# Optimization experiments

Measured on AMD Instinct MI355X. Metric: run time of the kernel, lower is better.

## Reference

```python
import jax, jax.numpy as jnp
import numpy as np

N = 50000      # nodes
E = 800000     # edges
IN_DIM = 16
D = 128        # latent_dim == d_model == num_heads*d_head
H = 8
DH = 16
DFF = 512
L = 3          # n_layers
CLAMP = 5.0
EPS = 1e-5


def _layer_norm(x, g, b):
    mu = jnp.mean(x, axis=-1, keepdims=True)
    var = jnp.mean((x - mu) ** 2, axis=-1, keepdims=True)
    return (x - mu) * jax.lax.rsqrt(var + EPS) * g + b


def setup_inputs() -> dict:
    key = jax.random.key(0)
    ks = jax.random.split(key, 16)
    def w(k, shape, fan_in):
        return jax.random.normal(k, shape, dtype=jnp.float32) * (1.0 / np.sqrt(fan_in))
    inp = {
        "nf": jax.random.normal(ks[0], (N, IN_DIM), dtype=jnp.float32),
        "src": jax.random.randint(ks[1], (E,), 0, N, dtype=jnp.int32),
        "dst": jax.random.randint(ks[2], (E,), 0, N, dtype=jnp.int32),
        "enc_W": w(ks[3], (D, IN_DIM), IN_DIM),
        "enc_b": jnp.zeros((D,), jnp.float32),
        "Wq": w(ks[4], (L, H * DH, D), D),
        "Wk": w(ks[5], (L, H * DH, D), D),
        "Wv": w(ks[6], (L, H * DH, D), D),
        "Wo": w(ks[7], (L, D, H * DH), H * DH),
        "ln1_g": jnp.ones((L, D), jnp.float32),
        "ln1_b": jnp.zeros((L, D), jnp.float32),
        "ffn_W1": w(ks[8], (L, DFF, D), D),
        "ffn_b1": jnp.zeros((L, DFF), jnp.float32),
        "ffn_W2": w(ks[9], (L, D, DFF), DFF),
        "ffn_b2": jnp.zeros((L, D), jnp.float32),
        "ln2_g": jnp.ones((L, D), jnp.float32),
        "ln2_b": jnp.zeros((L, D), jnp.float32),
        "dec_W": w(ks[10], (1, D), D),
        "dec_b": jnp.zeros((1,), jnp.float32),
    }
    return inp


def reference(nf, src, dst, enc_W, enc_b, Wq, Wk, Wv, Wo, ln1_g, ln1_b,
              ffn_W1, ffn_b1, ffn_W2, ffn_b2, ln2_g, ln2_b, dec_W, dec_b):
    h = nf @ enc_W.T + enc_b                       # [N, D]
    scale = 1.0 / np.sqrt(DH)
    for l in range(L):
        q = h @ Wq[l].T                            # [N, H*DH]
        k = h @ Wk[l].T
        v = h @ Wv[l].T
        qe = q[dst].reshape(E, H, DH)              # per-edge gather (dst query)
        ke = k[src].reshape(E, H, DH)
        u = jnp.sum(qe * ke, axis=-1) * scale      # [E, H]
        u = jnp.clip(u, -CLAMP, CLAMP)
        # edge_softmax: normalize over edges sharing the same dst node
        m = jax.ops.segment_max(u, dst, num_segments=N)   # [N, H]
        e = jnp.exp(u - m[dst])
        s = jax.ops.segment_sum(e, dst, num_segments=N)   # [N, H]
        a = e / s[dst]                             # [E, H]
        av = a[..., None] * v[src].reshape(E, H, DH)      # [E, H, DH]
        sum_av = jax.ops.segment_sum(av.reshape(E, H * DH), dst, num_segments=N)
        uh = sum_av @ Wo[l].T                      # [N, D]
        h1 = _layer_norm(h + uh, ln1_g[l], ln1_b[l])
        f = jax.nn.relu(h1 @ ffn_W1[l].T + ffn_b1[l]) @ ffn_W2[l].T + ffn_b2[l]
        h = _layer_norm(h1 + f, ln2_g[l], ln2_b[l])
    pred = h @ dec_W.T + dec_b                     # [N, 1]
    # BasicReadout('mean') over the single batched graph -> [1, 1]
    return jnp.mean(pred, axis=0, keepdims=True)
```

## Files before the change

kernel.cpp:

```cpp
#include <hip/hip_runtime.h>
#include <math.h>

static constexpr int D   = 128;
static constexpr int DFF = 512;
static constexpr int LAYERS = 3;
static constexpr float CLAMP_V = 5.0f;
static constexpr float LN_EPS = 1e-5f;

typedef unsigned short u16;
typedef unsigned int   u32;
typedef short bf16x8 __attribute__((ext_vector_type(8)));
typedef float f32x4  __attribute__((ext_vector_type(4)));

__device__ inline float4 ld4(const float* p){ return *reinterpret_cast<const float4*>(p); }
__device__ inline u16 f2bf(float f){ u32 u = __float_as_uint(f); return (u16)((u + 0x7fff + ((u>>16)&1)) >> 16); }
__device__ inline float bl(u32 u){ return __uint_as_float(u << 16); }
__device__ inline float bh(u32 u){ return __uint_as_float(u & 0xffff0000u); }

__device__ inline void gload_lds16(const void* g, void* l) {
  __builtin_amdgcn_global_load_lds(
      (const __attribute__((address_space(1))) void*)g,
      (__attribute__((address_space(3))) void*)l, 16, 0, 0);
}

__global__ __launch_bounds__(256) void count_kernel(const int* __restrict__ dst,
                                                    int* __restrict__ deg, int E)
{
  int e = blockIdx.x*256 + threadIdx.x;
  if (e < E) atomicAdd(&deg[dst[e]], 1);
}

__global__ __launch_bounds__(256) void scan_bsum(const int* __restrict__ deg,
                                                 int* __restrict__ bsum, int N)
{
  const int i0 = blockIdx.x*1024 + threadIdx.x*4;
  int s = 0;
  if (i0 + 3 < N) { int4 v = *(const int4*)&deg[i0]; s = v.x+v.y+v.z+v.w; }
  else { for (int t = 0; t < 4; t++) if (i0+t < N) s += deg[i0+t]; }
  #pragma unroll
  for (int off = 1; off < 64; off <<= 1) s += __shfl_xor(s, off);
  __shared__ int ws_[4];
  if ((threadIdx.x & 63) == 0) ws_[threadIdx.x >> 6] = s;
  __syncthreads();
  if (threadIdx.x == 0) bsum[blockIdx.x] = ws_[0]+ws_[1]+ws_[2]+ws_[3];
}

__global__ __launch_bounds__(64) void scan_bbase(int* __restrict__ bsum, int NB)
{
  const int tid = threadIdx.x;
  int base = 0;
  for (int c = 0; c < NB; c += 64) {
    const int idx = c + tid;
    int v = (idx < NB) ? bsum[idx] : 0;
    const int orig = v;
    #pragma unroll
    for (int off = 1; off < 64; off <<= 1) {
      int t = __shfl_up(v, off);
      if (tid >= off) v += t;
    }
    if (idx < NB) bsum[idx] = base + v - orig;
    base += __shfl(v, 63);
  }
}

__global__ __launch_bounds__(256) void scan_write(const int* __restrict__ deg,
    const int* __restrict__ bbase, int* __restrict__ offs, int* __restrict__ cursor, int N)
{
  const int i0 = blockIdx.x*1024 + threadIdx.x*4;
  int v[4] = {0,0,0,0};
  if (i0 + 3 < N) { int4 t = *(const int4*)&deg[i0]; v[0]=t.x; v[1]=t.y; v[2]=t.z; v[3]=t.w; }
  else { for (int t = 0; t < 4; t++) if (i0+t < N) v[t] = deg[i0+t]; }
  const int s = v[0]+v[1]+v[2]+v[3];
  const int lane = threadIdx.x & 63, w = threadIdx.x >> 6;
  int inc = s;
  #pragma unroll
  for (int off = 1; off < 64; off <<= 1) {
    int t = __shfl_up(inc, off);
    if (lane >= off) inc += t;
  }
  __shared__ int wsum[4];
  if (lane == 63) wsum[w] = inc;
  __syncthreads();
  int wb = 0;
  for (int t = 0; t < 4; t++) if (t < w) wb += wsum[t];
  int run = bbase[blockIdx.x] + wb + inc - s;
  #pragma unroll
  for (int t = 0; t < 4; t++) {
    if (i0 + t < N) { offs[i0+t] = run; cursor[i0+t] = run; run += v[t]; }
  }
  if (i0 <= N-1 && N-1 < i0+4) offs[N] = run;
}

__global__ __launch_bounds__(256) void fill_kernel(const int* __restrict__ dst,
    const int* __restrict__ src, int* __restrict__ cursor, int* __restrict__ csr_src, int E)
{
  int e = blockIdx.x*256 + threadIdx.x;
  if (e < E) {
    int p = atomicAdd(&cursor[dst[e]], 1);
    csr_src[p] = src[e];
  }
}

__global__ __launch_bounds__(256) void convert_weights(
    const float* __restrict__ Wq, const float* __restrict__ Wk, const float* __restrict__ Wv,
    const float* __restrict__ Wo, const float* __restrict__ W1, const float* __restrict__ W2,
    u16* __restrict__ out)
{
  const int SQKV = 3*384*128;
  const int SWO  = 3*128*128;
  const int SW1  = 3*512*128;
  const int SW2  = 3*128*512;
  int i = blockIdx.x*256 + threadIdx.x;
  if (i >= SQKV+SWO+SW1+SW2) return;
  float v;
  if (i < SQKV) {
    int l = i / (384*128), rem = i % (384*128);
    int row = rem / 128, col = rem % 128;
    const float* W = (row < 128) ? Wq : ((row < 256) ? Wk : Wv);
    v = W[(size_t)l*128*128 + (size_t)(row & 127)*128 + col];
  } else if (i < SQKV+SWO) {
    v = Wo[i - SQKV];
  } else if (i < SQKV+SWO+SW1) {
    v = W1[i - SQKV - SWO];
  } else {
    v = W2[i - SQKV - SWO - SW1];
  }
  out[i] = f2bf(v);
}

__global__ __launch_bounds__(256) void encoder_kernel(
    const float* __restrict__ nf, const float* __restrict__ W,
    const float* __restrict__ b, float* __restrict__ h, u16* __restrict__ hb, int N)
{
  int n = blockIdx.x*2 + (threadIdx.x >> 7);
  int d = threadIdx.x & 127;
  if (n >= N) return;
  const float* nr = nf + (size_t)n*16;
  const float* wr = W  + (size_t)d*16;
  float s = b[d];
  #pragma unroll
  for (int kk = 0; kk < 16; kk++) s = fmaf(nr[kk], wr[kk], s);
  h[(size_t)n*D + d]  = s;
  hb[(size_t)n*D + d] = f2bf(s);
}

template<int K>
__device__ inline void gemm_core(const u16* __restrict__ A, const u16* __restrict__ B,
                                 int M, int m0, u16* lA, u16* lB, f32x4 acc[4][4])
{
  const int tid  = threadIdx.x;
  const int lane = tid & 63;
  const int wid  = tid >> 6;
  const int wr   = wid >> 1, wc = wid & 1;

  const int ldrow = lane >> 3;
  const int gran  = (lane & 7) ^ ldrow;

  #pragma unroll
  for (int ks = 0; ks < K/64; ks++) {
    __syncthreads();
    const int k0 = ks*64 + gran*8;
    #pragma unroll
    for (int is = 0; is < 4; is++) {
      const int r  = wid*32 + is*8;
      int gm = m0 + r + ldrow; if (gm >= M) gm = M - 1;
      gload_lds16(A + (size_t)gm*K + k0, &lA[r*64]);
      gload_lds16(B + (size_t)(r + ldrow)*K + k0, &lB[r*64]);
    }
    asm volatile("s_waitcnt vmcnt(0)" ::: "memory");
    __syncthreads();

    #pragma unroll
    for (int k2 = 0; k2 < 2; k2++) {
      bf16x8 af[4], bfr[4];
      const int kq = k2*4 + (lane >> 4);
      #pragma unroll
      for (int mi = 0; mi < 4; mi++) {
        const int r = wr*64 + mi*16 + (lane & 15);
        af[mi] = *(const bf16x8*)&lA[r*64 + ((kq ^ (r & 7)) << 3)];
      }
      #pragma unroll
      for (int ni = 0; ni < 4; ni++) {
        const int r = wc*64 + ni*16 + (lane & 15);
        bfr[ni] = *(const bf16x8*)&lB[r*64 + ((kq ^ (r & 7)) << 3)];
      }
      #pragma unroll
      for (int mi = 0; mi < 4; mi++)
        #pragma unroll
        for (int ni = 0; ni < 4; ni++)
          acc[mi][ni] = __builtin_amdgcn_mfma_f32_16x16x32_bf16(af[mi], bfr[ni], acc[mi][ni], 0, 0, 0);
    }
  }
}

__global__ __launch_bounds__(256) void gemm_qkv(
    const u16* __restrict__ A, const u16* __restrict__ B,
    float* __restrict__ qf, u16* __restrict__ kvb, int M)
{
  __shared__ u16 lA[128*64];
  __shared__ u16 lB[128*64];
  const int s  = blockIdx.y;
  const int m0 = blockIdx.x * 128;
  f32x4 acc[4][4];
  #pragma unroll
  for (int i = 0; i < 4; i++)
    #pragma unroll
    for (int j = 0; j < 4; j++) { acc[i][j][0]=0.f; acc[i][j][1]=0.f; acc[i][j][2]=0.f; acc[i][j][3]=0.f; }

  gemm_core<128>(A, B + (size_t)s*128*128, M, m0, lA, lB, acc);

  const int lane  = threadIdx.x & 63;
  const int wid   = threadIdx.x >> 6;
  const int wr    = wid >> 1, wc = wid & 1;
  const int rbase = m0 + wr*64 + ((lane >> 4) << 2);
  const int cbase = wc*64 + (lane & 15);
  #pragma unroll
  for (int ni = 0; ni < 4; ni++) {
    const int col = cbase + ni*16;
    #pragma unroll
    for (int mi = 0; mi < 4; mi++) {
      #pragma unroll
      for (int r = 0; r < 4; r++) {
        const int gm = rbase + mi*16 + r;
        if (gm < M) {
          if (s == 0) qf[(size_t)gm*128 + col] = acc[mi][ni][r];
          else        kvb[(size_t)gm*256 + (s-1)*128 + col] = f2bf(acc[mi][ni][r]);
        }
      }
    }
  }
}

__global__ __launch_bounds__(256) void ffn_fused(
    const u16* __restrict__ savb, const u16* __restrict__ Wo,
    const u16* __restrict__ W1,   const u16* __restrict__ W2,
    const float* __restrict__ ln1g, const float* __restrict__ ln1b,
    const float* __restrict__ b1,   const float* __restrict__ b2,
    const float* __restrict__ ln2g, const float* __restrict__ ln2b,
    float* __restrict__ hf, u16* __restrict__ hb, int M)
{
  __shared__ u16 lA[64*64];
  __shared__ u16 lB[128*64];
  __shared__ u16 h1s[64*128];
  __shared__ u16 fs[64*128];
  __shared__ float lsum[64][2];
  __shared__ float lsq[64][2];

  const int tid  = threadIdx.x;
  const int lane = tid & 63;
  const int wid  = tid >> 6;
  const int wr   = wid >> 1, wc = wid & 1;
  const int m0   = blockIdx.x * 64;

  const int ldrow = lane >> 3;
  const int gran  = (lane & 7) ^ ldrow;

  const int rbase_l = wr*32 + ((lane >> 4) << 2);
  const int cbase   = wc*64 + (lane & 15);

  f32x4 acc1[2][4];
  #pragma unroll
  for (int i = 0; i < 2; i++)
    #pragma unroll
    for (int j = 0; j < 4; j++) { acc1[i][j][0]=0.f; acc1[i][j][1]=0.f; acc1[i][j][2]=0.f; acc1[i][j][3]=0.f; }

  #pragma unroll
  for (int ks = 0; ks < 2; ks++) {
    __syncthreads();
    const int k0 = ks*64 + gran*8;
    #pragma unroll
    for (int is = 0; is < 2; is++) {
      const int r = wid*16 + is*8;
      int gm = m0 + r + ldrow; if (gm >= M) gm = M - 1;
      gload_lds16(savb + (size_t)gm*128 + k0, &lA[r*64]);
    }
    #pragma unroll
    for (int is = 0; is < 4; is++) {
      const int r = wid*32 + is*8;
      gload_lds16(Wo + (size_t)(r + ldrow)*128 + k0, &lB[r*64]);
    }
    asm volatile("s_waitcnt vmcnt(0)" ::: "memory");
    __syncthreads();
    #pragma unroll
    for (int k2 = 0; k2 < 2; k2++) {
      const int kq = k2*4 + (lane >> 4);
      bf16x8 af[2], bfr[4];
      #pragma unroll
      for (int mi = 0; mi < 2; mi++) {
        const int r = wr*32 + mi*16 + (lane & 15);
        af[mi] = *(const bf16x8*)&lA[r*64 + ((kq ^ (r & 7)) << 3)];
      }
      #pragma unroll
      for (int ni = 0; ni < 4; ni++) {
        const int r = wc*64 + ni*16 + (lane & 15);
        bfr[ni] = *(const bf16x8*)&lB[r*64 + ((kq ^ (r & 7)) << 3)];
      }
      #pragma unroll
      for (int mi = 0; mi < 2; mi++)
        #pragma unroll
        for (int ni = 0; ni < 4; ni++)
          acc1[mi][ni] = __builtin_amdgcn_mfma_f32_16x16x32_bf16(af[mi], bfr[ni], acc1[mi][ni], 0, 0, 0);
    }
  }

  #pragma unroll
  for (int mi = 0; mi < 2; mi++) {
    #pragma unroll
    for (int r = 0; r < 4; r++) {
      const int lrow = rbase_l + mi*16 + r;
      int gr = m0 + lrow; if (gr >= M) gr = M - 1;
      float ps = 0.f, pq = 0.f;
      #pragma unroll
      for (int ni = 0; ni < 4; ni++) {
        const int col = cbase + ni*16;
        float x = acc1[mi][ni][r] + hf[(size_t)gr*128 + col];
        acc1[mi][ni][r] = x;
        ps += x; pq += x*x;
      }
      #pragma unroll
      for (int off = 1; off < 16; off <<= 1) { ps += __shfl_xor(ps, off); pq += __shfl_xor(pq, off); }
      if ((lane & 15) == 0) { lsum[lrow][wc] = ps; lsq[lrow][wc] = pq; }
    }
  }
  __syncthreads();
  #pragma unroll
  for (int mi = 0; mi < 2; mi++) {
    #pragma unroll
    for (int r = 0; r < 4; r++) {
      const int lrow = rbase_l + mi*16 + r;
      const float mean = (lsum[lrow][0] + lsum[lrow][1]) * (1.0f/128.0f);
      float var = (lsq[lrow][0] + lsq[lrow][1]) * (1.0f/128.0f) - mean*mean;
      const float rstd = rsqrtf(fmaxf(var, 0.f) + LN_EPS);
      #pragma unroll
      for (int ni = 0; ni < 4; ni++) {
        const int col = cbase + ni*16;
        float o = (acc1[mi][ni][r] - mean) * rstd * ln1g[col] + ln1b[col];
        acc1[mi][ni][r] = o;
        const int g16 = col >> 3;
        const int slot = ((g16 & 7) ^ (lrow & 7)) | (g16 & 8);
        h1s[lrow*128 + slot*8 + (col & 7)] = f2bf(o);
      }
    }
  }

  f32x4 acc3[2][4];
  #pragma unroll
  for (int i = 0; i < 2; i++)
    #pragma unroll
    for (int j = 0; j < 4; j++) { acc3[i][j][0]=0.f; acc3[i][j][1]=0.f; acc3[i][j][2]=0.f; acc3[i][j][3]=0.f; }

  for (int c = 0; c < 4; c++) {
    f32x4 acc2[2][4];
    #pragma unroll
    for (int i = 0; i < 2; i++)
      #pragma unroll
      for (int j = 0; j < 4; j++) { acc2[i][j][0]=0.f; acc2[i][j][1]=0.f; acc2[i][j][2]=0.f; acc2[i][j][3]=0.f; }

    #pragma unroll
    for (int s = 0; s < 2; s++) {
      __syncthreads();
      const int k0 = s*64 + gran*8;
      #pragma unroll
      for (int is = 0; is < 4; is++) {
        const int r = wid*32 + is*8;
        gload_lds16(W1 + (size_t)(c*128 + r + ldrow)*128 + k0, &lB[r*64]);
      }
      asm volatile("s_waitcnt vmcnt(0)" ::: "memory");
      __syncthreads();
      #pragma unroll
      for (int k2 = 0; k2 < 2; k2++) {
        const int kql = k2*4 + (lane >> 4);
        const int kqa = s*8 + kql;
        bf16x8 af[2], bfr[4];
        #pragma unroll
        for (int mi = 0; mi < 2; mi++) {
          const int r = wr*32 + mi*16 + (lane & 15);
          const int slot = ((kqa & 7) ^ (r & 7)) | (kqa & 8);
          af[mi] = *(const bf16x8*)&h1s[r*128 + slot*8];
        }
        #pragma unroll
        for (int ni = 0; ni < 4; ni++) {
          const int r = wc*64 + ni*16 + (lane & 15);
          bfr[ni] = *(const bf16x8*)&lB[r*64 + ((kql ^ (r & 7)) << 3)];
        }
        #pragma unroll
        for (int mi = 0; mi < 2; mi++)
          #pragma unroll
          for (int ni = 0; ni < 4; ni++)
            acc2[mi][ni] = __builtin_amdgcn_mfma_f32_16x16x32_bf16(af[mi], bfr[ni], acc2[mi][ni], 0, 0, 0);
      }
    }
    __syncthreads();
    #pragma unroll
    for (int mi = 0; mi < 2; mi++) {
      #pragma unroll
      for (int r = 0; r < 4; r++) {
        const int lrow = rbase_l + mi*16 + r;
        #pragma unroll
        for (int ni = 0; ni < 4; ni++) {
          const int col = cbase + ni*16;
          float v = fmaxf(acc2[mi][ni][r] + b1[c*128 + col], 0.f);
          const int g16 = col >> 3;
          const int slot = ((g16 & 7) ^ (lrow & 7)) | (g16 & 8);
          fs[lrow*128 + slot*8 + (col & 7)] = f2bf(v);
        }
      }
    }

    #pragma unroll
    for (int s = 0; s < 2; s++) {
      __syncthreads();
      const int k0 = s*64 + gran*8;
      #pragma unroll
      for (int is = 0; is < 4; is++) {
        const int r = wid*32 + is*8;
        gload_lds16(W2 + (size_t)(r + ldrow)*512 + c*128 + k0, &lB[r*64]);
      }
      asm volatile("s_waitcnt vmcnt(0)" ::: "memory");
      __syncthreads();
      #pragma unroll
      for (int k2 = 0; k2 < 2; k2++) {
        const int kql = k2*4 + (lane >> 4);
        const int kqa = s*8 + kql;
        bf16x8 af[2], bfr[4];
        #pragma unroll
        for (int mi = 0; mi < 2; mi++) {
          const int r = wr*32 + mi*16 + (lane & 15);
          const int slot = ((kqa & 7) ^ (r & 7)) | (kqa & 8);
          af[mi] = *(const bf16x8*)&fs[r*128 + slot*8];
        }
        #pragma unroll
        for (int ni = 0; ni < 4; ni++) {
          const int r = wc*64 + ni*16 + (lane & 15);
          bfr[ni] = *(const bf16x8*)&lB[r*64 + ((kql ^ (r & 7)) << 3)];
        }
        #pragma unroll
        for (int mi = 0; mi < 2; mi++)
          #pragma unroll
          for (int ni = 0; ni < 4; ni++)
            acc3[mi][ni] = __builtin_amdgcn_mfma_f32_16x16x32_bf16(af[mi], bfr[ni], acc3[mi][ni], 0, 0, 0);
      }
    }
  }

  #pragma unroll
  for (int mi = 0; mi < 2; mi++) {
    #pragma unroll
    for (int r = 0; r < 4; r++) {
      const int lrow = rbase_l + mi*16 + r;
      float ps = 0.f, pq = 0.f;
      #pragma unroll
      for (int ni = 0; ni < 4; ni++) {
        const int col = cbase + ni*16;
        float x = acc3[mi][ni][r] + b2[col] + acc1[mi][ni][r];
        acc3[mi][ni][r] = x;
        ps += x; pq += x*x;
      }
      #pragma unroll
      for (int off = 1; off < 16; off <<= 1) { ps += __shfl_xor(ps, off); pq += __shfl_xor(pq, off); }
      if ((lane & 15) == 0) { lsum[lrow][wc] = ps; lsq[lrow][wc] = pq; }
    }
  }
  __syncthreads();
  #pragma unroll
  for (int mi = 0; mi < 2; mi++) {
    #pragma unroll
    for (int r = 0; r < 4; r++) {
      const int lrow = rbase_l + mi*16 + r;
      const int grow = m0 + lrow;
      if (grow >= M) continue;
      const float mean = (lsum[lrow][0] + lsum[lrow][1]) * (1.0f/128.0f);
      float var = (lsq[lrow][0] + lsq[lrow][1]) * (1.0f/128.0f) - mean*mean;
      const float rstd = rsqrtf(fmaxf(var, 0.f) + LN_EPS);
      #pragma unroll
      for (int ni = 0; ni < 4; ni++) {
        const int col = cbase + ni*16;
        float o = (acc3[mi][ni][r] - mean) * rstd * ln2g[col] + ln2b[col];
        hf[(size_t)grow*128 + col] = o;
        hb[(size_t)grow*128 + col] = f2bf(o);
      }
    }
  }
}

__global__ __launch_bounds__(256) void attn_kernel(
    const float* __restrict__ q, const u16* __restrict__ kv,
    const int* __restrict__ offs, const int* __restrict__ csr_src,
    u16* __restrict__ outb, int N)
{
  const int tid = threadIdx.x;
  const int j   = tid & 15;
  const int n   = blockIdx.x*16 + (tid >> 4);
  if (n >= N) return;

  float qreg[8];
  *(float4*)&qreg[0] = ld4(&q[(size_t)n*128 + j*8]);
  *(float4*)&qreg[4] = ld4(&q[(size_t)n*128 + j*8 + 4]);

  const int start = offs[n];
  const int deg   = offs[n+1] - start;

  float s = 0.f;
  float acc[8] = {0,0,0,0,0,0,0,0};
  const int gb = tid & 48;

  for (int base = 0; base < deg; base += 16) {
    const int myidx = base + j;
    const int sn_mine = (myidx < deg) ? csr_src[start + myidx] : 0;
    const int cnt = (deg - base < 16) ? (deg - base) : 16;

    for (int b2 = 0; b2 < cnt; b2 += 4) {
      const int m4 = cnt - b2;
      uint4 K4[4], V4[4];
      #pragma unroll
      for (int u = 0; u < 4; u++) {
        const int sel = b2 + ((u < m4) ? u : 0);
        const int sn = __shfl(sn_mine, gb + sel);
        const u16* row = kv + (size_t)sn*256 + j*8;
        K4[u] = *(const uint4*)row;
        V4[u] = *(const uint4*)(row + 128);
      }
      #pragma unroll
      for (int u = 0; u < 4; u++) {
        if (u < m4) {
          float d = bl(K4[u].x)*qreg[0] + bh(K4[u].x)*qreg[1]
                  + bl(K4[u].y)*qreg[2] + bh(K4[u].y)*qreg[3]
                  + bl(K4[u].z)*qreg[4] + bh(K4[u].z)*qreg[5]
                  + bl(K4[u].w)*qreg[6] + bh(K4[u].w)*qreg[7];
          d += __shfl_xor(d, 1);
          float uu = fminf(fmaxf(d * 0.25f, -CLAMP_V), CLAMP_V);
          float e = __expf(uu - CLAMP_V);
          s += e;
          acc[0] = fmaf(e, bl(V4[u].x), acc[0]);
          acc[1] = fmaf(e, bh(V4[u].x), acc[1]);
          acc[2] = fmaf(e, bl(V4[u].y), acc[2]);
          acc[3] = fmaf(e, bh(V4[u].y), acc[3]);
          acc[4] = fmaf(e, bl(V4[u].z), acc[4]);
          acc[5] = fmaf(e, bh(V4[u].z), acc[5]);
          acc[6] = fmaf(e, bl(V4[u].w), acc[6]);
          acc[7] = fmaf(e, bh(V4[u].w), acc[7]);
        }
      }
    }
  }

  const float rs = (deg > 0) ? (1.0f / s) : 0.f;
  u16 o[8];
  #pragma unroll
  for (int t = 0; t < 8; t++) o[t] = f2bf(acc[t] * rs);
  *(uint4*)&outb[(size_t)n*128 + j*8] = *(const uint4*)o;
}

__global__ __launch_bounds__(256) void dec_partial(const float* __restrict__ h,
    const float* __restrict__ W, float* __restrict__ partials, int N)
{
  float acc = 0.f;
  for (int n = blockIdx.x*256 + threadIdx.x; n < N; n += 256*256) {
    const float* hr = h + (size_t)n*D;
    float s = 0.f;
    #pragma unroll
    for (int t = 0; t < 32; t++) {
      float4 hv = ld4(&hr[t*4]); float4 wv = ld4(&W[t*4]);
      s += hv.x*wv.x + hv.y*wv.y + hv.z*wv.z + hv.w*wv.w;
    }
    acc += s;
  }
  #pragma unroll
  for (int off = 1; off < 64; off <<= 1) acc += __shfl_xor(acc, off);
  __shared__ float red[4];
  int lane = threadIdx.x & 63, w = threadIdx.x >> 6;
  if (lane == 0) red[w] = acc;
  __syncthreads();
  if (threadIdx.x == 0) partials[blockIdx.x] = red[0]+red[1]+red[2]+red[3];
}

__global__ __launch_bounds__(256) void dec_final(const float* __restrict__ partials,
    const float* __restrict__ decb, float* __restrict__ out, int N)
{
  float a = partials[threadIdx.x];
  #pragma unroll
  for (int off = 1; off < 64; off <<= 1) a += __shfl_xor(a, off);
  __shared__ float red[4];
  int lane = threadIdx.x & 63, w = threadIdx.x >> 6;
  if (lane == 0) red[w] = a;
  __syncthreads();
  if (threadIdx.x == 0) out[0] = (red[0]+red[1]+red[2]+red[3]) / (float)N + decb[0];
}

extern "C" void kernel_launch(void* const* d_in, const int* in_sizes, int n_in,
                              void* d_out, int out_size, void* d_ws, size_t ws_size,
                              hipStream_t stream)
{
  const float* nf   = (const float*)d_in[0];
  const int*   src  = (const int*)  d_in[1];
  const int*   dst  = (const int*)  d_in[2];
  const float* encW = (const float*)d_in[3];
  const float* encb = (const float*)d_in[4];
  const float* Wq   = (const float*)d_in[5];
  const float* Wk   = (const float*)d_in[6];
  const float* Wv   = (const float*)d_in[7];
  const float* Wo   = (const float*)d_in[8];
  const float* ln1g = (const float*)d_in[9];
  const float* ln1b = (const float*)d_in[10];
  const float* W1   = (const float*)d_in[11];
  const float* b1   = (const float*)d_in[12];
  const float* W2   = (const float*)d_in[13];
  const float* b2   = (const float*)d_in[14];
  const float* ln2g = (const float*)d_in[15];
  const float* ln2b = (const float*)d_in[16];
  const float* decW = (const float*)d_in[17];
  const float* decb = (const float*)d_in[18];
  float* out = (float*)d_out;

  const int N = in_sizes[0] / 16;
  const int E = in_sizes[1];
  const int NB = (N + 1023) / 1024;

  float* ws   = (float*)d_ws;
  float* h    = ws;
  float* q    = h  + (size_t)N*128;
  u16*  hb    = (u16*)(q + (size_t)N*128);
  u16*  kvb   = hb  + (size_t)N*128;
  u16*  savb  = kvb + (size_t)N*256;
  int* deg    = (int*)(savb + (size_t)N*128);
  int* offs   = deg + N;
  int* cursor = offs + N + 1;
  int* csr    = cursor + N;
  int* bsum   = csr + E;
  float* partials = (float*)(bsum + ((NB + 255) & ~255));
  u16* wbuf   = (u16*)(partials + 512);
  u16* wqkv   = wbuf;
  u16* wo_b   = wbuf + 147456;
  u16* w1_b   = wbuf + 196608;
  u16* w2_b   = wbuf + 393216;

  hipMemsetAsync(deg, 0, sizeof(int)*N, stream);
  count_kernel<<<(E+255)/256, 256, 0, stream>>>(dst, deg, E);
  scan_bsum<<<NB, 256, 0, stream>>>(deg, bsum, N);
  scan_bbase<<<1, 64, 0, stream>>>(bsum, NB);
  scan_write<<<NB, 256, 0, stream>>>(deg, bsum, offs, cursor, N);
  fill_kernel<<<(E+255)/256, 256, 0, stream>>>(dst, src, cursor, csr, E);

  convert_weights<<<(589824+255)/256, 256, 0, stream>>>(Wq, Wk, Wv, Wo, W1, W2, wbuf);

  encoder_kernel<<<(N+1)/2, 256, 0, stream>>>(nf, encW, encb, h, hb, N);

  const int gmx = (N + 127)/128;
  for (int l = 0; l < LAYERS; l++) {
    const u16* wqkv_l = wqkv + (size_t)l*384*128;
    const u16* wo_l   = wo_b + (size_t)l*128*128;
    const u16* w1_l   = w1_b + (size_t)l*512*128;
    const u16* w2_l   = w2_b + (size_t)l*128*512;

    gemm_qkv<<<dim3(gmx,3), 256, 0, stream>>>(hb, wqkv_l, q, kvb, N);

    attn_kernel<<<(N+15)/16, 256, 0, stream>>>(q, kvb, offs, csr, savb, N);

    ffn_fused<<<(N+63)/64, 256, 0, stream>>>(
        savb, wo_l, w1_l, w2_l,
        ln1g + l*D, ln1b + l*D, b1 + l*DFF, b2 + l*D, ln2g + l*D, ln2b + l*D,
        h, hb, N);
  }

  dec_partial<<<256, 256, 0, stream>>>(h, decW, partials, N);
  dec_final<<<1, 256, 0, stream>>>(partials, decb, out, N);
}
```

Baseline: 567.6 us.

## Double-buffer LDS loads in QKV and FFN GEMMs; widen edge gather batch

```diff
diff --git a/kernel.cpp b/kernel.cpp
--- a/kernel.cpp
+++ b/kernel.cpp
@@ -144,52 +144,55 @@
   hb[(size_t)n*D + d] = f2bf(s);
 }
 
-template<int K>
-__device__ inline void gemm_core(const u16* __restrict__ A, const u16* __restrict__ B,
-                                 int M, int m0, u16* lA, u16* lB, f32x4 acc[4][4])
-{
-  const int tid  = threadIdx.x;
-  const int lane = tid & 63;
-  const int wid  = tid >> 6;
-  const int wr   = wid >> 1, wc = wid & 1;
-
-  const int ldrow = lane >> 3;
-  const int gran  = (lane & 7) ^ ldrow;
-
-  #pragma unroll
-  for (int ks = 0; ks < K/64; ks++) {
-    __syncthreads();
-    const int k0 = ks*64 + gran*8;
-    #pragma unroll
-    for (int is = 0; is < 4; is++) {
-      const int r  = wid*32 + is*8;
-      int gm = m0 + r + ldrow; if (gm >= M) gm = M - 1;
-      gload_lds16(A + (size_t)gm*K + k0, &lA[r*64]);
-      gload_lds16(B + (size_t)(r + ldrow)*K + k0, &lB[r*64]);
-    }
-    asm volatile("s_waitcnt vmcnt(0)" ::: "memory");
-    __syncthreads();
-
-    #pragma unroll
-    for (int k2 = 0; k2 < 2; k2++) {
-      bf16x8 af[4], bfr[4];
-      const int kq = k2*4 + (lane >> 4);
-      #pragma unroll
-      for (int mi = 0; mi < 4; mi++) {
-        const int r = wr*64 + mi*16 + (lane & 15);
-        af[mi] = *(const bf16x8*)&lA[r*64 + ((kq ^ (r & 7)) << 3)];
-      }
-      #pragma unroll
-      for (int ni = 0; ni < 4; ni++) {
-        const int r = wc*64 + ni*16 + (lane & 15);
-        bfr[ni] = *(const bf16x8*)&lB[r*64 + ((kq ^ (r & 7)) << 3)];
-      }
-      #pragma unroll
-      for (int mi = 0; mi < 4; mi++)
-        #pragma unroll
-        for (int ni = 0; ni < 4; ni++)
-          acc[mi][ni] = __builtin_amdgcn_mfma_f32_16x16x32_bf16(af[mi], bfr[ni], acc[mi][ni], 0, 0, 0);
-    }
+__device__ inline void mfma_step128(const u16* __restrict__ la, const u16* __restrict__ lb,
+                                    int lane, int wr, int wc, f32x4 (&acc)[4][4])
+{
+  #pragma unroll
+  for (int k2 = 0; k2 < 2; k2++) {
+    bf16x8 af[4], bfr[4];
+    const int kq = k2*4 + (lane >> 4);
+    #pragma unroll
+    for (int mi = 0; mi < 4; mi++) {
+      const int r = wr*64 + mi*16 + (lane & 15);
+      af[mi] = *(const bf16x8*)&la[r*64 + ((kq ^ (r & 7)) << 3)];
+    }
+    #pragma unroll
+    for (int ni = 0; ni < 4; ni++) {
+      const int r = wc*64 + ni*16 + (lane & 15);
+      bfr[ni] = *(const bf16x8*)&lb[r*64 + ((kq ^ (r & 7)) << 3)];
+    }
+    #pragma unroll
+    for (int mi = 0; mi < 4; mi++)
+      #pragma unroll
+      for (int ni = 0; ni < 4; ni++)
+        acc[mi][ni] = __builtin_amdgcn_mfma_f32_16x16x32_bf16(af[mi], bfr[ni], acc[mi][ni], 0, 0, 0);
+  }
+}
+
+__device__ inline void mfma_stage64(const u16* __restrict__ Atile, const u16* __restrict__ Btile,
+                                    int lane, int wr, int wc, int kabase, f32x4 (&acc)[2][4])
+{
+  #pragma unroll
+  for (int k2 = 0; k2 < 2; k2++) {
+    const int kql = k2*4 + (lane >> 4);
+    const int kqa = kabase + kql;
+    bf16x8 af[2], bfr[4];
+    #pragma unroll
+    for (int mi = 0; mi < 2; mi++) {
+      const int r = wr*32 + mi*16 + (lane & 15);
+      const int slot = ((kqa & 7) ^ (r & 7)) | (kqa & 8);
+      af[mi] = *(const bf16x8*)&Atile[r*128 + slot*8];
+    }
+    #pragma unroll
+    for (int ni = 0; ni < 4; ni++) {
+      const int r = wc*64 + ni*16 + (lane & 15);
+      bfr[ni] = *(const bf16x8*)&Btile[r*64 + ((kql ^ (r & 7)) << 3)];
+    }
+    #pragma unroll
+    for (int mi = 0; mi < 2; mi++)
+      #pragma unroll
+      for (int ni = 0; ni < 4; ni++)
+        acc[mi][ni] = __builtin_amdgcn_mfma_f32_16x16x32_bf16(af[mi], bfr[ni], acc[mi][ni], 0, 0, 0);
   }
 }
 
@@ -197,21 +200,42 @@
     const u16* __restrict__ A, const u16* __restrict__ B,
     float* __restrict__ qf, u16* __restrict__ kvb, int M)
 {
-  __shared__ u16 lA[128*64];
-  __shared__ u16 lB[128*64];
-  const int s  = blockIdx.y;
+  __shared__ u16 lA[2][128*64];
+  __shared__ u16 lB[2][128*64];
+  const int sY = blockIdx.y;
   const int m0 = blockIdx.x * 128;
+  const int tid = threadIdx.x, lane = tid & 63, wid = tid >> 6;
+  const int wr = wid >> 1, wc = wid & 1;
+  const int ldrow = lane >> 3;
+  const int gran  = (lane & 7) ^ ldrow;
+  const u16* Bm = B + (size_t)sY*128*128;
+
   f32x4 acc[4][4];
   #pragma unroll
   for (int i = 0; i < 4; i++)
     #pragma unroll
     for (int j = 0; j < 4; j++) { acc[i][j][0]=0.f; acc[i][j][1]=0.f; acc[i][j][2]=0.f; acc[i][j][3]=0.f; }
 
-  gemm_core<128>(A, B + (size_t)s*128*128, M, m0, lA, lB, acc);
-
-  const int lane  = threadIdx.x & 63;
-  const int wid   = threadIdx.x >> 6;
-  const int wr    = wid >> 1, wc = wid & 1;
+  auto issue = [&](int ks) {
+    const int k0 = ks*64 + gran*8;
+    #pragma unroll
+    for (int is = 0; is < 4; is++) {
+      const int r = wid*32 + is*8;
+      int gm = m0 + r + ldrow; if (gm >= M) gm = M - 1;
+      gload_lds16(A + (size_t)gm*128 + k0, &lA[ks][r*64]);
+      gload_lds16(Bm + (size_t)(r + ldrow)*128 + k0, &lB[ks][r*64]);
+    }
+  };
+
+  issue(0);
+  asm volatile("s_waitcnt vmcnt(0)" ::: "memory");
+  __syncthreads();
+  issue(1);
+  mfma_step128(lA[0], lB[0], lane, wr, wc, acc);
+  asm volatile("s_waitcnt vmcnt(0)" ::: "memory");
+  __syncthreads();
+  mfma_step128(lA[1], lB[1], lane, wr, wc, acc);
+
   const int rbase = m0 + wr*64 + ((lane >> 4) << 2);
   const int cbase = wc*64 + (lane & 15);
   #pragma unroll
@@ -223,8 +247,8 @@
       for (int r = 0; r < 4; r++) {
         const int gm = rbase + mi*16 + r;
         if (gm < M) {
-          if (s == 0) qf[(size_t)gm*128 + col] = acc[mi][ni][r];
-          else        kvb[(size_t)gm*256 + (s-1)*128 + col] = f2bf(acc[mi][ni][r]);
+          if (sY == 0) qf[(size_t)gm*128 + col] = acc[mi][ni][r];
+          else         kvb[(size_t)gm*256 + (sY-1)*128 + col] = f2bf(acc[mi][ni][r]);
         }
       }
     }
@@ -239,8 +263,7 @@
     const float* __restrict__ ln2g, const float* __restrict__ ln2b,
     float* __restrict__ hf, u16* __restrict__ hb, int M)
 {
-  __shared__ u16 lA[64*64];
-  __shared__ u16 lB[128*64];
+  __shared__ u16 lB[2][128*64];
   __shared__ u16 h1s[64*128];
   __shared__ u16 fs[64*128];
   __shared__ float lsum[64][2];
@@ -258,188 +281,124 @@
   const int rbase_l = wr*32 + ((lane >> 4) << 2);
   const int cbase   = wc*64 + (lane & 15);
 
-  f32x4 acc1[2][4];
-  #pragma unroll
-  for (int i = 0; i < 2; i++)
-    #pragma unroll
-    for (int j = 0; j < 4; j++) { acc1[i][j][0]=0.f; acc1[i][j][1]=0.f; acc1[i][j][2]=0.f; acc1[i][j][3]=0.f; }
-
-  #pragma unroll
-  for (int ks = 0; ks < 2; ks++) {
-    __syncthreads();
-    const int k0 = ks*64 + gran*8;
-    #pragma unroll
-    for (int is = 0; is < 2; is++) {
-      const int r = wid*16 + is*8;
-      int gm = m0 + r + ldrow; if (gm >= M) gm = M - 1;
-      gload_lds16(savb + (size_t)gm*128 + k0, &lA[r*64]);
-    }
+  auto stage_issue = [&](int s) {
+    u16* dst = lB[s & 1];
     #pragma unroll
     for (int is = 0; is < 4; is++) {
       const int r = wid*32 + is*8;
-      gload_lds16(Wo + (size_t)(r + ldrow)*128 + k0, &lB[r*64]);
-    }
-    asm volatile("s_waitcnt vmcnt(0)" ::: "memory");
-    __syncthreads();
-    #pragma unroll
-    for (int k2 = 0; k2 < 2; k2++) {
-      const int kq = k2*4 + (lane >> 4);
-      bf16x8 af[2], bfr[4];
+      const u16* gp;
+      if (s < 2) gp = Wo + (size_t)(r + ldrow)*128 + s*64;
+      else {
+        const int t = s - 2, c = t >> 2, k = t & 3;
+        gp = (k < 2) ? (W1 + (size_t)(c*128 + r + ldrow)*128 + k*64)
+                     : (W2 + (size_t)(r + ldrow)*512 + c*128 + (k-2)*64);
+      }
+      gload_lds16(gp + gran*8, dst + r*64);
+    }
+  };
+
+  #pragma unroll
+  for (int is = 0; is < 4; is++) {
+    const int r0 = wid*16 + is*4;
+    const int rr = r0 + (lane >> 4);
+    int gm = m0 + rr; if (gm >= M) gm = M - 1;
+    const int gsrc = ((lane & 7) ^ (rr & 7)) | (lane & 8);
+    gload_lds16(savb + (size_t)gm*128 + gsrc*8, &fs[r0*128]);
+  }
+  stage_issue(0);
+
+  f32x4 acc1[2][4], acc2[2][4], acc3[2][4];
+  #pragma unroll
+  for (int i = 0; i < 2; i++)
+    #pragma unroll
+    for (int j = 0; j < 4; j++) {
+      acc1[i][j][0]=0.f; acc1[i][j][1]=0.f; acc1[i][j][2]=0.f; acc1[i][j][3]=0.f;
+      acc3[i][j][0]=0.f; acc3[i][j][1]=0.f; acc3[i][j][2]=0.f; acc3[i][j][3]=0.f;
+    }
+
+  asm volatile("s_waitcnt vmcnt(0)" ::: "memory");
+  __syncthreads();
+
+  #pragma unroll
+  for (int s = 0; s < 18; s++) {
+    if (s < 17) stage_issue(s + 1);
+
+    if (s >= 2 && ((s - 2) & 3) == 0) {
+      #pragma unroll
+      for (int i = 0; i < 2; i++)
+        #pragma unroll
+        for (int j = 0; j < 4; j++) { acc2[i][j][0]=0.f; acc2[i][j][1]=0.f; acc2[i][j][2]=0.f; acc2[i][j][3]=0.f; }
+    }
+
+    if (s < 2)
+      mfma_stage64(fs,  lB[s & 1], lane, wr, wc, (s & 1)*8, acc1);
+    else if (((s - 2) & 3) < 2)
+      mfma_stage64(h1s, lB[s & 1], lane, wr, wc, (s & 1)*8, acc2);
+    else
+      mfma_stage64(fs,  lB[s & 1], lane, wr, wc, (s & 1)*8, acc3);
+
+    if (s == 1) {
       #pragma unroll
       for (int mi = 0; mi < 2; mi++) {
-        const int r = wr*32 + mi*16 + (lane & 15);
-        af[mi] = *(const bf16x8*)&lA[r*64 + ((kq ^ (r & 7)) << 3)];
-      }
-      #pragma unroll
-      for (int ni = 0; ni < 4; ni++) {
-        const int r = wc*64 + ni*16 + (lane & 15);
-        bfr[ni] = *(const bf16x8*)&lB[r*64 + ((kq ^ (r & 7)) << 3)];
-      }
-      #pragma unroll
-      for (int mi = 0; mi < 2; mi++)
         #pragma unroll
-        for (int ni = 0; ni < 4; ni++)
-          acc1[mi][ni] = __builtin_amdgcn_mfma_f32_16x16x32_bf16(af[mi], bfr[ni], acc1[mi][ni], 0, 0, 0);
-    }
-  }
-
-  #pragma unroll
-  for (int mi = 0; mi < 2; mi++) {
-    #pragma unroll
-    for (int r = 0; r < 4; r++) {
-      const int lrow = rbase_l + mi*16 + r;
-      int gr = m0 + lrow; if (gr >= M) gr = M - 1;
-      float ps = 0.f, pq = 0.f;
-      #pragma unroll
-      for (int ni = 0; ni < 4; ni++) {
-        const int col = cbase + ni*16;
-        float x = acc1[mi][ni][r] + hf[(size_t)gr*128 + col];
-        acc1[mi][ni][r] = x;
-        ps += x; pq += x*x;
-      }
-      #pragma unroll
-      for (int off = 1; off < 16; off <<= 1) { ps += __shfl_xor(ps, off); pq += __shfl_xor(pq, off); }
-      if ((lane & 15) == 0) { lsum[lrow][wc] = ps; lsq[lrow][wc] = pq; }
-    }
-  }
-  __syncthreads();
-  #pragma unroll
-  for (int mi = 0; mi < 2; mi++) {
-    #pragma unroll
-    for (int r = 0; r < 4; r++) {
-      const int lrow = rbase_l + mi*16 + r;
-      const float mean = (lsum[lrow][0] + lsum[lrow][1]) * (1.0f/128.0f);
-      float var = (lsq[lrow][0] + lsq[lrow][1]) * (1.0f/128.0f) - mean*mean;
-      const float rstd = rsqrtf(fmaxf(var, 0.f) + LN_EPS);
-      #pragma unroll
-      for (int ni = 0; ni < 4; ni++) {
-        const int col = cbase + ni*16;
-        float o = (acc1[mi][ni][r] - mean) * rstd * ln1g[col] + ln1b[col];
-        acc1[mi][ni][r] = o;
-        const int g16 = col >> 3;
-        const int slot = ((g16 & 7) ^ (lrow & 7)) | (g16 & 8);
-        h1s[lrow*128 + slot*8 + (col & 7)] = f2bf(o);
-      }
-    }
-  }
-
-  f32x4 acc3[2][4];
-  #pragma unroll
-  for (int i = 0; i < 2; i++)
-    #pragma unroll
-    for (int j = 0; j < 4; j++) { acc3[i][j][0]=0.f; acc3[i][j][1]=0.f; acc3[i][j][2]=0.f; acc3[i][j][3]=0.f; }
-
-  for (int c = 0; c < 4; c++) {
-    f32x4 acc2[2][4];
-    #pragma unroll
-    for (int i = 0; i < 2; i++)
-      #pragma unroll
-      for (int j = 0; j < 4; j++) { acc2[i][j][0]=0.f; acc2[i][j][1]=0.f; acc2[i][j][2]=0.f; acc2[i][j][3]=0.f; }
-
-    #pragma unroll
-    for (int s = 0; s < 2; s++) {
+        for (int r = 0; r < 4; r++) {
+          const int lrow = rbase_l + mi*16 + r;
+          int gr = m0 + lrow; if (gr >= M) gr = M - 1;
+          float ps = 0.f, pq = 0.f;
+          #pragma unroll
+          for (int ni = 0; ni < 4; ni++) {
+            const int col = cbase + ni*16;
+            float x = acc1[mi][ni][r] + hf[(size_t)gr*128 + col];
+            acc1[mi][ni][r] = x;
+            ps += x; pq += x*x;
+          }
+          #pragma unroll
+          for (int off = 1; off < 16; off <<= 1) { ps += __shfl_xor(ps, off); pq += __shfl_xor(pq, off); }
+          if ((lane & 15) == 0) { lsum[lrow][wc] = ps; lsq[lrow][wc] = pq; }
+        }
+      }
       __syncthreads();
-      const int k0 = s*64 + gran*8;
-      #pragma unroll
-      for (int is = 0; is < 4; is++) {
-        const int r = wid*32 + is*8;
-        gload_lds16(W1 + (size_t)(c*128 + r + ldrow)*128 + k0, &lB[r*64]);
-      }
+      #pragma unroll
+      for (int mi = 0; mi < 2; mi++) {
+        #pragma unroll
+        for (int r = 0; r < 4; r++) {
+          const int lrow = rbase_l + mi*16 + r;
+          const float mean = (lsum[lrow][0] + lsum[lrow][1]) * (1.0f/128.0f);
+          float var = (lsq[lrow][0] + lsq[lrow][1]) * (1.0f/128.0f) - mean*mean;
+          const float rstd = rsqrtf(fmaxf(var, 0.f) + LN_EPS);
+          #pragma unroll
+          for (int ni = 0; ni < 4; ni++) {
+            const int col = cbase + ni*16;
+            float o = (acc1[mi][ni][r] - mean) * rstd * ln1g[col] + ln1b[col];
+            acc1[mi][ni][r] = o;
+            const int g16 = col >> 3;
+            const int slot = ((g16 & 7) ^ (lrow & 7)) | (g16 & 8);
+            h1s[lrow*128 + slot*8 + (col & 7)] = f2bf(o);
+          }
+        }
+      }
+    } else if (s >= 2 && ((s - 2) & 3) == 1) {
+      const int c = (s - 2) >> 2;
+      #pragma unroll
+      for (int mi = 0; mi < 2; mi++) {
+        #pragma unroll
+        for (int r = 0; r < 4; r++) {
+          const int lrow = rbase_l + mi*16 + r;
+          #pragma unroll
+          for (int ni = 0; ni < 4; ni++) {
+            const int col = cbase + ni*16;
+            float v = fmaxf(acc2[mi][ni][r] + b1[c*128 + col], 0.f);
+            const int g16 = col >> 3;
+            const int slot = ((g16 & 7) ^ (lrow & 7)) | (g16 & 8);
+            fs[lrow*128 + slot*8 + (col & 7)] = f2bf(v);
+          }
+        }
+      }
+    }
+
+    if (s < 17) {
       asm volatile("s_waitcnt vmcnt(0)" ::: "memory");
       __syncthreads();
-      #pragma unroll
-      for (int k2 = 0; k2 < 2; k2++) {
-        const int kql = k2*4 + (lane >> 4);
-        const int kqa = s*8 + kql;
-        bf16x8 af[2], bfr[4];
-        #pragma unroll
-        for (int mi = 0; mi < 2; mi++) {
-          const int r = wr*32 + mi*16 + (lane & 15);
-          const int slot = ((kqa & 7) ^ (r & 7)) | (kqa & 8);
-          af[mi] = *(const bf16x8*)&h1s[r*128 + slot*8];
-        }
-        #pragma unroll
-        for (int ni = 0; ni < 4; ni++) {
-          const int r = wc*64 + ni*16 + (lane & 15);
-          bfr[ni] = *(const bf16x8*)&lB[r*64 + ((kql ^ (r & 7)) << 3)];
-        }
-        #pragma unroll
-        for (int mi = 0; mi < 2; mi++)
-          #pragma unroll
-          for (int ni = 0; ni < 4; ni++)
-            acc2[mi][ni] = __builtin_amdgcn_mfma_f32_16x16x32_bf16(af[mi], bfr[ni], acc2[mi][ni], 0, 0, 0);
-      }
-    }
-    __syncthreads();
-    #pragma unroll
-    for (int mi = 0; mi < 2; mi++) {
-      #pragma unroll
-      for (int r = 0; r < 4; r++) {
-        const int lrow = rbase_l + mi*16 + r;
-        #pragma unroll
-        for (int ni = 0; ni < 4; ni++) {
-          const int col = cbase + ni*16;
-          float v = fmaxf(acc2[mi][ni][r] + b1[c*128 + col], 0.f);
-          const int g16 = col >> 3;
-          const int slot = ((g16 & 7) ^ (lrow & 7)) | (g16 & 8);
-          fs[lrow*128 + slot*8 + (col & 7)] = f2bf(v);
-        }
-      }
-    }
-
-    #pragma unroll
-    for (int s = 0; s < 2; s++) {
-      __syncthreads();
-      const int k0 = s*64 + gran*8;
-      #pragma unroll
-      for (int is = 0; is < 4; is++) {
-        const int r = wid*32 + is*8;
-        gload_lds16(W2 + (size_t)(r + ldrow)*512 + c*128 + k0, &lB[r*64]);
-      }
-      asm volatile("s_waitcnt vmcnt(0)" ::: "memory");
-      __syncthreads();
-      #pragma unroll
-      for (int k2 = 0; k2 < 2; k2++) {
-        const int kql = k2*4 + (lane >> 4);
-        const int kqa = s*8 + kql;
-        bf16x8 af[2], bfr[4];
-        #pragma unroll
-        for (int mi = 0; mi < 2; mi++) {
-          const int r = wr*32 + mi*16 + (lane & 15);
-          const int slot = ((kqa & 7) ^ (r & 7)) | (kqa & 8);
-          af[mi] = *(const bf16x8*)&fs[r*128 + slot*8];
-        }
-        #pragma unroll
-        for (int ni = 0; ni < 4; ni++) {
-          const int r = wc*64 + ni*16 + (lane & 15);
-          bfr[ni] = *(const bf16x8*)&lB[r*64 + ((kql ^ (r & 7)) << 3)];
-        }
-        #pragma unroll
-        for (int mi = 0; mi < 2; mi++)
-          #pragma unroll
-          for (int ni = 0; ni < 4; ni++)
-            acc3[mi][ni] = __builtin_amdgcn_mfma_f32_16x16x32_bf16(af[mi], bfr[ni], acc3[mi][ni], 0, 0, 0);
-      }
     }
   }
 
@@ -509,20 +468,20 @@
     const int sn_mine = (myidx < deg) ? csr_src[start + myidx] : 0;
     const int cnt = (deg - base < 16) ? (deg - base) : 16;
 
-    for (int b2 = 0; b2 < cnt; b2 += 4) {
-      const int m4 = cnt - b2;
-      uint4 K4[4], V4[4];
-      #pragma unroll
-      for (int u = 0; u < 4; u++) {
-        const int sel = b2 + ((u < m4) ? u : 0);
+    for (int b2 = 0; b2 < cnt; b2 += 8) {
+      const int m8 = cnt - b2;
+      uint4 K4[8], V4[8];
+      #pragma unroll
+      for (int u = 0; u < 8; u++) {
+        const int sel = b2 + ((u < m8) ? u : 0);
         const int sn = __shfl(sn_mine, gb + sel);
         const u16* row = kv + (size_t)sn*256 + j*8;
         K4[u] = *(const uint4*)row;
         V4[u] = *(const uint4*)(row + 128);
       }
       #pragma unroll
-      for (int u = 0; u < 4; u++) {
-        if (u < m4) {
+      for (int u = 0; u < 8; u++) {
+        if (u < m8) {
           float d = bl(K4[u].x)*qreg[0] + bh(K4[u].x)*qreg[1]
                   + bl(K4[u].y)*qreg[2] + bh(K4[u].y)*qreg[3]
                   + bl(K4[u].z)*qreg[4] + bh(K4[u].z)*qreg[5]
```

Measured after the change: 556.4 us. 1.02x faster.
